# Kernel optimization log

Hardware: AMD Instinct MI355X
Metric: run time of the kernel (lower is better)

The kernel has to match this reference:

```python
import jax, jax.numpy as jnp
import numpy as np

MARGIN = 0.3
NEG_FILL = 1e9  # larger than any real distance; keeps min-reduction valid


def setup_inputs() -> dict:
    key = jax.random.key(0)
    k1, k2 = jax.random.split(key)
    embeddings = jax.random.normal(k1, (4096, 256), dtype=jnp.float32)
    labels = jax.random.randint(k2, (4096,), 0, 512, dtype=jnp.int64)
    return {"embeddings": embeddings, "labels": labels}


def _pairwise_distances(embeddings):
    # Faithful to the torch version, including the zero-distance sqrt guard.
    dot = jnp.matmul(embeddings, embeddings.T)          # [B, B]
    sq = jnp.diagonal(dot)                              # [B]
    d2 = sq[None, :] - 2.0 * dot + sq[:, None]
    d2 = jnp.maximum(d2, 0.0)
    zero_mask = (d2 == 0.0).astype(embeddings.dtype)
    d = jnp.sqrt(d2 + zero_mask * 1e-16)
    return d * (1.0 - zero_mask)


def reference(embeddings, labels):
    B = labels.shape[0]
    d = _pairwise_distances(embeddings)                 # [B, B]

    same = labels[:, None] == labels[None, :]           # [B, B]
    eye = jnp.eye(B, dtype=bool)
    pos_mask = same & ~eye
    neg_mask = ~same

    has_pos = jnp.any(pos_mask, axis=1)
    has_neg = jnp.any(neg_mask, axis=1)
    valid = has_pos & has_neg                           # [B]

    # Row-wise masked reductions (distances >= 0 so -1 is a safe max fill).
    hardest_pos = jnp.max(jnp.where(pos_mask, d, -1.0), axis=1)
    hardest_neg = jnp.min(jnp.where(neg_mask, d, NEG_FILL), axis=1)

    per_anchor = jnp.maximum(hardest_pos - hardest_neg + MARGIN, 0.0)
    n_valid = jnp.sum(valid.astype(jnp.float32))
    total = jnp.sum(jnp.where(valid, per_anchor, 0.0))
    return jnp.where(n_valid > 0, total / jnp.maximum(n_valid, 1.0), 0.0)
```

## Files before the change

kernel.cpp:

```cpp
#include <hip/hip_runtime.h>
#include <hip/hip_fp16.h>

#define BN 4096
#define DIM 256
#define NBLK 32
#define NPAIR 528
#define MARGIN_F 0.3f
#define NEG_FILL_F 1e9f
#define HP_SENT_BITS 0xBF800000

typedef __attribute__((ext_vector_type(8))) _Float16 f16x8;
typedef __attribute__((ext_vector_type(4))) float f32x4;

__global__ __launch_bounds__(256) void tl_prep(const float* __restrict__ E,
                                               float* __restrict__ norms,
                                               float* __restrict__ red,
                                               ushort* __restrict__ Eh) {
    __shared__ ushort sh[4][272];
    const int tid  = threadIdx.x;
    const int lane = tid & 63;
    const int wrow = tid >> 6;
    const int row0 = blockIdx.x * 4;
    const int row  = row0 + wrow;

    float4 v = reinterpret_cast<const float4*>(E + (size_t)row * DIM)[lane];
    float f[4] = {v.x, v.y, v.z, v.w};
    ushort hb[4];
    float s = 0.0f;
    #pragma unroll
    for (int q = 0; q < 4; ++q) {
        s += f[q] * f[q];
        hb[q] = __half_as_ushort(__float2half(f[q]));
    }
    *reinterpret_cast<ushort4*>(&sh[wrow][lane * 4]) = make_ushort4(hb[0], hb[1], hb[2], hb[3]);

    #pragma unroll
    for (int m = 32; m; m >>= 1) s += __shfl_xor(s, m, 64);
    if (lane == 0) norms[row] = s;
    if (blockIdx.x == 0 && tid < 3) red[tid] = 0.0f;

    __syncthreads();
    if (tid < 128) {
        const int kc = tid >> 2, r = tid & 3;
        const f16x8 frag = *reinterpret_cast<const f16x8*>(&sh[r][kc * 8]);
        *reinterpret_cast<f16x8*>(Eh + (((size_t)(kc * BN + row0 + r)) << 3)) = frag;
    }
}

__global__ __launch_bounds__(256, 3) void tl_main(const ushort* __restrict__ Eh,
                                                  const int* __restrict__ labels,
                                                  const float* __restrict__ norms,
                                                  float* __restrict__ pHP,
                                                  float* __restrict__ pHN) {
    __shared__ int comb[512];

    const int tid  = threadIdx.x;
    const int lane = tid & 63;
    const int wave = tid >> 6;
    const int wy = wave >> 1, wx = wave & 1;
    const int quad = lane >> 4, l15 = lane & 15;

    int t = blockIdx.x, ib = 0, off = 0;
    while (off + (NBLK - ib) <= t) { off += NBLK - ib; ++ib; }
    const int jb = ib + (t - off);
    const int i0 = ib * 128, j0 = jb * 128;

    f32x4 acc[4][4];
    #pragma unroll
    for (int r = 0; r < 4; ++r)
        #pragma unroll
        for (int c = 0; c < 4; ++c)
            acc[r][c] = (f32x4){0.f, 0.f, 0.f, 0.f};

    const ushort* baseQ = Eh + (size_t)quad * (BN * 8);
    int rA[4], rB[4];
    #pragma unroll
    for (int r = 0; r < 4; ++r) rA[r] = (i0 + wy * 64 + r * 16 + l15) * 8;
    #pragma unroll
    for (int c = 0; c < 4; ++c) rB[c] = (j0 + wx * 64 + c * 16 + l15) * 8;

    f16x8 a0[4], b0[4], a1[4], b1[4];
    auto LD = [&](f16x8 (&A)[4], f16x8 (&B)[4], int s) {
        const size_t so = (size_t)s * (4u * BN * 8u);
        #pragma unroll
        for (int r = 0; r < 4; ++r)
            A[r] = *reinterpret_cast<const f16x8*>(baseQ + so + (size_t)rA[r]);
        #pragma unroll
        for (int c = 0; c < 4; ++c)
            B[c] = *reinterpret_cast<const f16x8*>(baseQ + so + (size_t)rB[c]);
    };
    auto MM = [&](f16x8 (&A)[4], f16x8 (&B)[4]) {
        #pragma unroll
        for (int c = 0; c < 4; ++c)
            #pragma unroll
            for (int r = 0; r < 4; ++r)
                acc[r][c] = __builtin_amdgcn_mfma_f32_16x16x32_f16(A[r], B[c], acc[r][c], 0, 0, 0);
    };

    LD(a0, b0, 0);
    LD(a1, b1, 1); MM(a0, b0);
    LD(a0, b0, 2); MM(a1, b1);
    LD(a1, b1, 3); MM(a0, b0);
    LD(a0, b0, 4); MM(a1, b1);
    LD(a1, b1, 5); MM(a0, b0);
    LD(a0, b0, 6); MM(a1, b1);
    LD(a1, b1, 7); MM(a0, b0);
    MM(a1, b1);

    const int rowBase = i0 + wy * 64;
    const int colBase = j0 + wx * 64;

    float nrow[4][4]; int lrow[4][4];
    #pragma unroll
    for (int r = 0; r < 4; ++r)
        #pragma unroll
        for (int e = 0; e < 4; ++e) {
            const int g = rowBase + r * 16 + quad * 4 + e;
            nrow[r][e] = norms[g];
            lrow[r][e] = labels[g];
        }
    float ncol[4]; int lcol[4];
    #pragma unroll
    for (int c = 0; c < 4; ++c) {
        const int g = colBase + c * 16 + l15;
        ncol[c] = norms[g];
        lcol[c] = labels[g];
    }

    float rmax[4][4], rmin[4][4], cmax[4], cmin[4];
    #pragma unroll
    for (int r = 0; r < 4; ++r)
        #pragma unroll
        for (int e = 0; e < 4; ++e) { rmax[r][e] = -1.0f; rmin[r][e] = NEG_FILL_F; }
    #pragma unroll
    for (int c = 0; c < 4; ++c) { cmax[c] = -1.0f; cmin[c] = NEG_FILL_F; }

    #pragma unroll
    for (int c = 0; c < 4; ++c) {
        const int gcol = colBase + c * 16 + l15;
        #pragma unroll
        for (int r = 0; r < 4; ++r) {
            #pragma unroll
            for (int e = 0; e < 4; ++e) {
                const int grow = rowBase + r * 16 + quad * 4 + e;
                float d2 = nrow[r][e] + ncol[c] - 2.0f * acc[r][c][e];
                d2 = fmaxf(d2, 0.0f);
                if (lrow[r][e] == lcol[c]) {
                    if (grow != gcol) {
                        rmax[r][e] = fmaxf(rmax[r][e], d2);
                        cmax[c]    = fmaxf(cmax[c], d2);
                    }
                } else {
                    rmin[r][e] = fminf(rmin[r][e], d2);
                    cmin[c]    = fminf(cmin[c], d2);
                }
            }
        }
    }

    #pragma unroll
    for (int m = 1; m <= 8; m <<= 1) {
        #pragma unroll
        for (int r = 0; r < 4; ++r)
            #pragma unroll
            for (int e = 0; e < 4; ++e) {
                rmax[r][e] = fmaxf(rmax[r][e], __shfl_xor(rmax[r][e], m, 64));
                rmin[r][e] = fminf(rmin[r][e], __shfl_xor(rmin[r][e], m, 64));
            }
    }
    #pragma unroll
    for (int m = 16; m <= 32; m <<= 1) {
        #pragma unroll
        for (int c = 0; c < 4; ++c) {
            cmax[c] = fmaxf(cmax[c], __shfl_xor(cmax[c], m, 64));
            cmin[c] = fminf(cmin[c], __shfl_xor(cmin[c], m, 64));
        }
    }

    int*      srhp = comb;
    unsigned* srhn = reinterpret_cast<unsigned*>(comb + 128);
    int*      schp = comb + 256;
    unsigned* schn = reinterpret_cast<unsigned*>(comb + 384);
    if (tid < 128) {
        srhp[tid] = (int)HP_SENT_BITS;
        srhn[tid] = __float_as_uint(NEG_FILL_F);
        schp[tid] = (int)HP_SENT_BITS;
        schn[tid] = __float_as_uint(NEG_FILL_F);
    }
    __syncthreads();
    if (l15 == 0) {
        #pragma unroll
        for (int r = 0; r < 4; ++r)
            #pragma unroll
            for (int e = 0; e < 4; ++e) {
                const int lr = wy * 64 + r * 16 + quad * 4 + e;
                atomicMax(&srhp[lr], __float_as_int(rmax[r][e]));
                atomicMin(&srhn[lr], __float_as_uint(rmin[r][e]));
            }
    }
    if (quad == 0) {
        #pragma unroll
        for (int c = 0; c < 4; ++c) {
            const int lc = wx * 64 + c * 16 + l15;
            atomicMax(&schp[lc], __float_as_int(cmax[c]));
            atomicMin(&schn[lc], __float_as_uint(cmin[c]));
        }
    }
    __syncthreads();
    if (tid < 128) {
        float rp = __int_as_float(srhp[tid]);
        float rn = __uint_as_float(srhn[tid]);
        const float cp = __int_as_float(schp[tid]);
        const float cn = __uint_as_float(schn[tid]);
        if (ib == jb) {
            pHP[(size_t)jb * BN + i0 + tid] = fmaxf(rp, cp);
            pHN[(size_t)jb * BN + i0 + tid] = fminf(rn, cn);
        } else {
            pHP[(size_t)jb * BN + i0 + tid] = rp;
            pHN[(size_t)jb * BN + i0 + tid] = rn;
            pHP[(size_t)ib * BN + j0 + tid] = cp;
            pHN[(size_t)ib * BN + j0 + tid] = cn;
        }
    }
}

__global__ __launch_bounds__(256) void tl_reduce(const float* __restrict__ pHP,
                                                 const float* __restrict__ pHN,
                                                 float* __restrict__ red,
                                                 float* __restrict__ out) {
    __shared__ float shp[4][64], shn[4][64];
    const int rl = threadIdx.x & 63;
    const int g  = threadIdx.x >> 6;
    const int i  = blockIdx.x * 64 + rl;
    float hp2 = -1.0f, hn2 = NEG_FILL_F;
    #pragma unroll
    for (int q = 0; q < 8; ++q) {
        const int s = g * 8 + q;
        hp2 = fmaxf(hp2, pHP[(size_t)s * BN + i]);
        hn2 = fminf(hn2, pHN[(size_t)s * BN + i]);
    }
    shp[g][rl] = hp2;
    shn[g][rl] = hn2;
    __syncthreads();
    if (g == 0) {
        #pragma unroll
        for (int k = 1; k < 4; ++k) {
            hp2 = fmaxf(hp2, shp[k][rl]);
            hn2 = fminf(hn2, shn[k][rl]);
        }
        const bool valid = (hp2 >= 0.0f) && (hn2 < NEG_FILL_F);
        const float hp = sqrtf(fmaxf(hp2, 0.0f));
        const float hn = sqrtf(hn2);
        const float per = fmaxf(hp - hn + MARGIN_F, 0.0f);
        float s_ = valid ? per : 0.0f;
        float c_ = valid ? 1.0f : 0.0f;
        #pragma unroll
        for (int m = 32; m; m >>= 1) {
            s_ += __shfl_xor(s_, m, 64);
            c_ += __shfl_xor(c_, m, 64);
        }
        if (rl == 0) {
            atomicAdd(&red[0], s_);
            atomicAdd(&red[1], c_);
            __threadfence();
            const unsigned ticket = atomicAdd(reinterpret_cast<unsigned*>(&red[2]), 1u);
            if (ticket == gridDim.x - 1) {
                const float S2 = atomicAdd(&red[0], 0.0f);
                const float C2 = atomicAdd(&red[1], 0.0f);
                out[0] = (C2 > 0.0f) ? (S2 / fmaxf(C2, 1.0f)) : 0.0f;
            }
        }
    }
}

extern "C" void kernel_launch(void* const* d_in, const int* in_sizes, int n_in,
                              void* d_out, int out_size, void* d_ws, size_t ws_size,
                              hipStream_t stream) {
    const float* E      = (const float*)d_in[0];
    const int*   labels = (const int*)d_in[1];

    float*  ws    = (float*)d_ws;
    float*  norms = ws;
    float*  red   = ws + 4096;
    float*  pHP   = ws + 8192;
    float*  pHN   = ws + 8192 + NBLK * BN;
    ushort* Eh    = (ushort*)(ws + 8192 + 2 * NBLK * BN);

    tl_prep<<<BN / 4, 256, 0, stream>>>(E, norms, red, Eh);
    tl_main<<<NPAIR, 256, 0, stream>>>(Eh, labels, norms, pHP, pHN);
    tl_reduce<<<BN / 64, 256, 0, stream>>>(pHP, pHN, red, (float*)d_out);
}
```

Measured before the change: 80.42 us.

## Fuse final reduction into main kernel via global atomics and last-block ticket

```diff
diff --git a/kernel.cpp b/kernel.cpp
--- a/kernel.cpp
+++ b/kernel.cpp
@@ -15,6 +15,8 @@
 __global__ __launch_bounds__(256) void tl_prep(const float* __restrict__ E,
                                                float* __restrict__ norms,
                                                float* __restrict__ red,
+                                               int* __restrict__ hp2i,
+                                               unsigned* __restrict__ hn2u,
                                                ushort* __restrict__ Eh) {
     __shared__ ushort sh[4][272];
     const int tid  = threadIdx.x;
@@ -37,6 +39,10 @@
     #pragma unroll
     for (int m = 32; m; m >>= 1) s += __shfl_xor(s, m, 64);
     if (lane == 0) norms[row] = s;
+    if (tid < 4) {
+        hp2i[row0 + tid] = (int)HP_SENT_BITS;
+        hn2u[row0 + tid] = __float_as_uint(NEG_FILL_F);
+    }
     if (blockIdx.x == 0 && tid < 3) red[tid] = 0.0f;
 
     __syncthreads();
@@ -50,9 +56,13 @@
 __global__ __launch_bounds__(256, 3) void tl_main(const ushort* __restrict__ Eh,
                                                   const int* __restrict__ labels,
                                                   const float* __restrict__ norms,
-                                                  float* __restrict__ pHP,
-                                                  float* __restrict__ pHN) {
+                                                  int* __restrict__ hp2i,
+                                                  unsigned* __restrict__ hn2u,
+                                                  float* __restrict__ red,
+                                                  float* __restrict__ out) {
     __shared__ int comb[512];
+    __shared__ unsigned lastFlag;
+    __shared__ float redS[4], redC[4];
 
     const int tid  = threadIdx.x;
     const int lane = tid & 63;
@@ -208,67 +218,55 @@
     }
     __syncthreads();
     if (tid < 128) {
-        float rp = __int_as_float(srhp[tid]);
-        float rn = __uint_as_float(srhn[tid]);
-        const float cp = __int_as_float(schp[tid]);
-        const float cn = __uint_as_float(schn[tid]);
+        int      rp = srhp[tid];
+        unsigned rn = srhn[tid];
+        const int      cp = schp[tid];
+        const unsigned cn = schn[tid];
         if (ib == jb) {
-            pHP[(size_t)jb * BN + i0 + tid] = fmaxf(rp, cp);
-            pHN[(size_t)jb * BN + i0 + tid] = fminf(rn, cn);
+            rp = max(rp, cp);
+            rn = min(rn, cn);
+            if (rp != (int)HP_SENT_BITS) atomicMax(&hp2i[i0 + tid], rp);
+            atomicMin(&hn2u[i0 + tid], rn);
         } else {
-            pHP[(size_t)jb * BN + i0 + tid] = rp;
-            pHN[(size_t)jb * BN + i0 + tid] = rn;
-            pHP[(size_t)ib * BN + j0 + tid] = cp;
-            pHN[(size_t)ib * BN + j0 + tid] = cn;
-        }
-    }
-}
-
-__global__ __launch_bounds__(256) void tl_reduce(const float* __restrict__ pHP,
-                                                 const float* __restrict__ pHN,
-                                                 float* __restrict__ red,
-                                                 float* __restrict__ out) {
-    __shared__ float shp[4][64], shn[4][64];
-    const int rl = threadIdx.x & 63;
-    const int g  = threadIdx.x >> 6;
-    const int i  = blockIdx.x * 64 + rl;
-    float hp2 = -1.0f, hn2 = NEG_FILL_F;
-    #pragma unroll
-    for (int q = 0; q < 8; ++q) {
-        const int s = g * 8 + q;
-        hp2 = fmaxf(hp2, pHP[(size_t)s * BN + i]);
-        hn2 = fminf(hn2, pHN[(size_t)s * BN + i]);
-    }
-    shp[g][rl] = hp2;
-    shn[g][rl] = hn2;
-    __syncthreads();
-    if (g == 0) {
-        #pragma unroll
-        for (int k = 1; k < 4; ++k) {
-            hp2 = fmaxf(hp2, shp[k][rl]);
-            hn2 = fminf(hn2, shn[k][rl]);
-        }
-        const bool valid = (hp2 >= 0.0f) && (hn2 < NEG_FILL_F);
-        const float hp = sqrtf(fmaxf(hp2, 0.0f));
-        const float hn = sqrtf(hn2);
-        const float per = fmaxf(hp - hn + MARGIN_F, 0.0f);
-        float s_ = valid ? per : 0.0f;
-        float c_ = valid ? 1.0f : 0.0f;
+            if (rp != (int)HP_SENT_BITS) atomicMax(&hp2i[i0 + tid], rp);
+            atomicMin(&hn2u[i0 + tid], rn);
+            if (cp != (int)HP_SENT_BITS) atomicMax(&hp2i[j0 + tid], cp);
+            atomicMin(&hn2u[j0 + tid], cn);
+        }
+    }
+
+    __threadfence();
+    __syncthreads();
+    if (tid == 0) {
+        const unsigned ticket = atomicAdd(reinterpret_cast<unsigned*>(&red[2]), 1u);
+        lastFlag = (ticket == NPAIR - 1) ? 1u : 0u;
+    }
+    __syncthreads();
+    if (lastFlag) {
+        float s_ = 0.0f, c_ = 0.0f;
+        #pragma unroll
+        for (int q = 0; q < BN / 256; ++q) {
+            const int r = q * 256 + tid;
+            const int      hpB = atomicMax(&hp2i[r], (int)0x80000000);
+            const unsigned hnB = atomicMin(&hn2u[r], 0xFFFFFFFFu);
+            const float hp2 = __int_as_float(hpB);
+            const float hn2 = __uint_as_float(hnB);
+            if (hp2 >= 0.0f && hn2 < NEG_FILL_F) {
+                s_ += fmaxf(sqrtf(hp2) - sqrtf(hn2) + MARGIN_F, 0.0f);
+                c_ += 1.0f;
+            }
+        }
         #pragma unroll
         for (int m = 32; m; m >>= 1) {
             s_ += __shfl_xor(s_, m, 64);
             c_ += __shfl_xor(c_, m, 64);
         }
-        if (rl == 0) {
-            atomicAdd(&red[0], s_);
-            atomicAdd(&red[1], c_);
-            __threadfence();
-            const unsigned ticket = atomicAdd(reinterpret_cast<unsigned*>(&red[2]), 1u);
-            if (ticket == gridDim.x - 1) {
-                const float S2 = atomicAdd(&red[0], 0.0f);
-                const float C2 = atomicAdd(&red[1], 0.0f);
-                out[0] = (C2 > 0.0f) ? (S2 / fmaxf(C2, 1.0f)) : 0.0f;
-            }
+        if (lane == 0) { redS[wave] = s_; redC[wave] = c_; }
+        __syncthreads();
+        if (tid == 0) {
+            const float S = redS[0] + redS[1] + redS[2] + redS[3];
+            const float C = redC[0] + redC[1] + redC[2] + redC[3];
+            out[0] = (C > 0.0f) ? (S / fmaxf(C, 1.0f)) : 0.0f;
         }
     }
 }
@@ -279,14 +277,13 @@
     const float* E      = (const float*)d_in[0];
     const int*   labels = (const int*)d_in[1];
 
-    float*  ws    = (float*)d_ws;
-    float*  norms = ws;
-    float*  red   = ws + 4096;
-    float*  pHP   = ws + 8192;
-    float*  pHN   = ws + 8192 + NBLK * BN;
-    ushort* Eh    = (ushort*)(ws + 8192 + 2 * NBLK * BN);
-
-    tl_prep<<<BN / 4, 256, 0, stream>>>(E, norms, red, Eh);
-    tl_main<<<NPAIR, 256, 0, stream>>>(Eh, labels, norms, pHP, pHN);
-    tl_reduce<<<BN / 64, 256, 0, stream>>>(pHP, pHN, red, (float*)d_out);
+    float*    ws    = (float*)d_ws;
+    float*    norms = ws;
+    float*    red   = ws + 4096;
+    int*      hp2i  = (int*)(ws + 8192);
+    unsigned* hn2u  = (unsigned*)(ws + 12288);
+    ushort*   Eh    = (ushort*)(ws + 16384);
+
+    tl_prep<<<BN / 4, 256, 0, stream>>>(E, norms, red, hp2i, hn2u, Eh);
+    tl_main<<<NPAIR, 256, 0, stream>>>(Eh, labels, norms, hp2i, hn2u, red, (float*)d_out);
 }
```

Measured after the change: 106.9 us. 1.33x slower.
